# Optimization experiments

Measured on AMD Instinct MI355X. Metric: run time of the kernel, lower is better.

The kernel has to match this reference:

```python
import jax, jax.numpy as jnp
import numpy as np

T, B, F, H, O = 512, 1024, 16, 32, 8  # seq_len, batch, input_size, hidden, classes


def setup_inputs() -> dict:
    key = jax.random.key(0)
    ks = jax.random.split(key, 11)
    s = 1.0 / np.sqrt(H)  # PyTorch LSTM/Linear uniform init scale
    u = lambda k, shp: jax.random.uniform(k, shp, jnp.float32, -s, s)
    return {
        "x": jax.random.normal(ks[0], (T, B, F), jnp.float32),
        "W_ih_f": u(ks[1], (4 * H, F)),
        "W_hh_f": u(ks[2], (4 * H, H)),
        "b_f": u(ks[3], (4 * H,)),  # combined b_ih + b_hh
        "W_ih_b": u(ks[4], (4 * H, F)),
        "W_hh_b": u(ks[5], (4 * H, H)),
        "b_b": u(ks[6], (4 * H,)),
        "W_fc_h": u(ks[7], (O, 2 * H)),
        "b_fc_h": u(ks[8], (O,)),
        "W_fc_o": jax.random.uniform(ks[9], (O, B * O), jnp.float32, -1 / np.sqrt(B * O), 1 / np.sqrt(B * O)),
        "b_fc_o": u(ks[10], (O,)),
    }


def _lstm_final_hidden(x, W_ih, W_hh, b):
    """Run one LSTM direction over x:(T,B,F); return final hidden h:(B,H)."""
    h_dim = W_hh.shape[1]
    # precompute input contribution for all timesteps: (T, B, 4H)
    gates_x = jnp.einsum('tbf,gf->tbg', x, W_ih) + b

    def step(carry, gx):
        h, c = carry
        g = gx + h @ W_hh.T  # (B, 4H), PyTorch gate order i,f,g,o
        i, f, gg, o = jnp.split(g, 4, axis=-1)
        c = jax.nn.sigmoid(f) * c + jax.nn.sigmoid(i) * jnp.tanh(gg)
        h = jax.nn.sigmoid(o) * jnp.tanh(c)
        return (h, c), None

    bsz = x.shape[1]
    init = (jnp.zeros((bsz, h_dim), x.dtype), jnp.zeros((bsz, h_dim), x.dtype))
    (h, _), _ = jax.lax.scan(step, init, gates_x)
    return h


def reference(x, W_ih_f, W_hh_f, b_f, W_ih_b, W_hh_b, b_b,
              W_fc_h, b_fc_h, W_fc_o, b_fc_o):
    h_fwd = _lstm_final_hidden(x, W_ih_f, W_hh_f, b_f)          # hidden_state[-2]
    h_bwd = _lstm_final_hidden(x[::-1], W_ih_b, W_hh_b, b_b)    # hidden_state[-1]
    hidden = jnp.concatenate([h_fwd, h_bwd], axis=1)            # (B, 2H)
    hidden_fc = hidden @ W_fc_h.T + b_fc_h                      # (B, O)
    flat = hidden_fc.reshape(-1)                                # (B*O,) == flat_dim
    out = W_fc_o @ flat + b_fc_o                                # (O,)
    return jax.nn.softmax(out)
```

## Files before the change

kernel.cpp:

```cpp
#include <hip/hip_runtime.h>

#define TT 512
#define BB 1024
#define FF 16
#define HH 32
#define OO 8
#define CH 16
#define NC (TT / CH)
#define NG 128

typedef _Float16 f16;
typedef f16 v2h __attribute__((ext_vector_type(2)));
typedef f16 v4h __attribute__((ext_vector_type(4)));
typedef f16 v8h __attribute__((ext_vector_type(8)));
typedef float f32x4 __attribute__((ext_vector_type(4)));
typedef int   v2i  __attribute__((ext_vector_type(2)));

__device__ __forceinline__ float rcp_fast(float x) { return __builtin_amdgcn_rcpf(x); }
__device__ __forceinline__ float sigm2(float y) {
    return rcp_fast(1.0f + __builtin_amdgcn_exp2f(-y));
}
__device__ __forceinline__ float fdot2(v2h a, v2h b, float c) {
    return __builtin_amdgcn_fdot2(a, b, c, false);
}
__device__ __forceinline__ v2h i2h(int s) { return __builtin_bit_cast(v2h, s); }

__device__ __forceinline__ float xhalf_swap(float v) {
#if __has_builtin(__builtin_amdgcn_permlane32_swap)
    int pi = __float_as_int(v);
    v2i sw = __builtin_amdgcn_permlane32_swap(pi, pi, false, false);
    return __int_as_float(sw.x);
#else
    return __shfl_xor(v, 32);
#endif
}

#define LSTEP(tt)                                                              \
  {                                                                            \
    const int xm = ((tt) & 7) << 2;                                            \
    const float gx0 = gxc[(tt) * NG + (r0 ^ xm)];                              \
    const float gx1 = gxc[(tt) * NG + (r1 ^ xm)];                              \
    float B0 = fdot2(i2h(hs[0]), w0h[0], pb0);                                 \
    float B1 = fdot2(i2h(hs[0]), w1h[0], pb1);                                 \
    float C0 = fdot2(i2h(hs[8]), w0h[8], gx0);                                 \
    float C1 = fdot2(i2h(hs[8]), w1h[8], gx1);                                 \
    _Pragma("unroll")                                                          \
    for (int j = 1; j < 8; ++j) {                                              \
      B0 = fdot2(i2h(hs[j]),     w0h[j],     B0);                              \
      B1 = fdot2(i2h(hs[j]),     w1h[j],     B1);                              \
      C0 = fdot2(i2h(hs[8 + j]), w0h[8 + j], C0);                              \
      C1 = fdot2(i2h(hs[8 + j]), w1h[8 + j], C1);                              \
    }                                                                          \
    const float g0 = B0 + C0;                                                  \
    const float g1 = B1 + C1;                                                  \
    const float s0 = sigm2(g0);                         \
    const float s1 = fmaf(sigm2(g1), pm, pa);           \
    const float prod = s0 * s1;                                                \
    const float recv = xhalf_swap(prod);                                       \
    c = fmaf(s0, c, recv);                               \
    const float th = fmaf(2.0f, sigm2(L2E2 * c), -1.0f);                       \
    h = s1 * th;                                           \
    const int hn = __builtin_amdgcn_mov_dpp(__float_as_int(h),                 \
                                            0xB1, 0xF, 0xF, true);             \
    auto pk = __builtin_amdgcn_cvt_pkrtz(h, __int_as_float(hn));               \
    const int pki = __builtin_bit_cast(int, pk);                               \
    _Pragma("unroll")                                                          \
    for (int m = 0; m < HH / 2; ++m)                                           \
      hs[m] = __builtin_amdgcn_readlane(pki, 32 + 2 * m);                      \
  }

__global__ __launch_bounds__(64, 2)
void lstm_seq_kernel(const float* __restrict__ x,
                     const float* __restrict__ Wih_f, const float* __restrict__ Whh_f,
                     const float* __restrict__ b_f,
                     const float* __restrict__ Wih_b, const float* __restrict__ Whh_b,
                     const float* __restrict__ b_b,
                     float* __restrict__ hidden)
{
    const int bid  = blockIdx.x;
    const int dir  = bid >> 10;
    const int bb   = bid & (BB - 1);
    const int lane = threadIdx.x;
    const int hi   = lane >> 5;
    const int kk   = lane & 31;

    const float* __restrict__ Wih  = dir ? Wih_b : Wih_f;
    const float* __restrict__ Whh  = dir ? Whh_b : Whh_f;
    const float* __restrict__ bias = dir ? b_b   : b_f;

    const float LOG2E = 1.4426950408889634f;
    const float L2E2  = 2.0f * LOG2E;

    const int r0 = kk + hi * HH;
    const int r1 = r0 + 2 * HH;
    const float sc0 = LOG2E;
    const float sc1 = hi ? LOG2E : L2E2;
    const float pm = hi ? 1.0f : 2.0f;
    const float pa = hi ? 0.0f : -1.0f;

    v2h w0h[HH / 2], w1h[HH / 2];
#pragma unroll
    for (int q = 0; q < HH / 4; ++q) {
        float4 a = ((const float4*)(Whh + r0 * HH))[q];
        w0h[2*q]   = (v2h){(f16)(a.x * sc0), (f16)(a.y * sc0)};
        w0h[2*q+1] = (v2h){(f16)(a.z * sc0), (f16)(a.w * sc0)};
        float4 b2 = ((const float4*)(Whh + r1 * HH))[q];
        w1h[2*q]   = (v2h){(f16)(b2.x * sc1), (f16)(b2.y * sc1)};
        w1h[2*q+1] = (v2h){(f16)(b2.z * sc1), (f16)(b2.w * sc1)};
    }
    const float pb0 = bias[r0] * sc0;
    const float pb1 = bias[r1] * sc1;

    v8h awx[8];
#pragma unroll
    for (int T = 0; T < 8; ++T) {
        v8h t = {(f16)0,(f16)0,(f16)0,(f16)0,(f16)0,(f16)0,(f16)0,(f16)0};
        if (lane < 32) {
            const int gate = T * 16 + (lane & 15);
            const float sc = (gate >= 64 && gate < 96) ? L2E2 : LOG2E;
            const float* wrow = Wih + gate * FF + (lane >> 4) * 8;
#pragma unroll
            for (int j = 0; j < 8; ++j) t[j] = (f16)(wrow[j] * sc);
        }
        awx[T] = t;
    }

    __shared__ __align__(16) f16   xsb[2 * CH * FF];
    __shared__ __align__(16) float gxb[2 * CH * NG];

    const int sl = lane >> 2;
    const int wl = lane & 3;
    const int t0 = dir ? (TT - 1 - sl) : sl;
    const float* xp = x + (size_t)t0 * (BB * FF) + (size_t)bb * FF + wl * 4;
    const ptrdiff_t dstep = (dir ? -(ptrdiff_t)CH : (ptrdiff_t)CH) * (BB * FF);

    const int mst = lane & 15;
    const int mq  = (lane >> 4) * 4;
    const int mxr = (mst & 7) << 2;

    {
        float4 f0 = *(const float4*)xp;
        *(v4h*)(xsb + sl * FF + wl * 4) =
            (v4h){(f16)f0.x, (f16)f0.y, (f16)f0.z, (f16)f0.w};
    }
    xp += dstep;
    {
        v8h bx0 = {(f16)0,(f16)0,(f16)0,(f16)0,(f16)0,(f16)0,(f16)0,(f16)0};
        if (lane < 32)
            bx0 = *(const v8h*)(xsb + (lane & 15) * FF + (lane >> 4) * 8);
        float* gw = gxb + mst * NG;
#pragma unroll
        for (int T = 0; T < 8; ++T) {
            f32x4 acc = __builtin_amdgcn_mfma_f32_16x16x32_f16(
                awx[T], bx0, (f32x4){0.f, 0.f, 0.f, 0.f}, 0, 0, 0);
            *(f32x4*)(gw + ((mq + T * 16) ^ mxr)) = acc;
        }
    }
    float4 nf = *(const float4*)xp;
    xp += dstep;

    float c = 0.0f, h = 0.0f;
    int hs[HH / 2];
#pragma unroll
    for (int m = 0; m < HH / 2; ++m) hs[m] = 0;

    for (int ci = 0; ci < NC; ++ci) {
        const int bufc = ci & 1;
        const int bufn = bufc ^ 1;
        const bool more = (ci + 1 < NC);

        v8h bx = {(f16)0,(f16)0,(f16)0,(f16)0,(f16)0,(f16)0,(f16)0,(f16)0};
        if (more) {
            *(v4h*)(xsb + bufn * (CH * FF) + sl * FF + wl * 4) =
                (v4h){(f16)nf.x, (f16)nf.y, (f16)nf.z, (f16)nf.w};
            if (lane < 32)
                bx = *(const v8h*)(xsb + bufn * (CH * FF) + (lane & 15) * FF + (lane >> 4) * 8);
            if (ci + 2 < NC) { nf = *(const float4*)xp; xp += dstep; }
        }

        const float* gxc = gxb + bufc * (CH * NG);

#pragma unroll
        for (int tt = 0; tt < 12; ++tt) LSTEP(tt)

        if (more) {
            float* gw = gxb + bufn * (CH * NG) + mst * NG;
#pragma unroll
            for (int T = 0; T < 8; ++T) {
                f32x4 acc = __builtin_amdgcn_mfma_f32_16x16x32_f16(
                    awx[T], bx, (f32x4){0.f, 0.f, 0.f, 0.f}, 0, 0, 0);
                *(f32x4*)(gw + ((mq + T * 16) ^ mxr)) = acc;
            }
        }

#pragma unroll
        for (int tt = 12; tt < CH; ++tt) LSTEP(tt)
    }

    if (hi) hidden[(size_t)bb * 64 + dir * HH + kk] = h;
}

__global__ __launch_bounds__(256)
void fc_partial_kernel(const float* __restrict__ hidden,
                       const float* __restrict__ Wfh, const float* __restrict__ bfh,
                       const float* __restrict__ Wfo,
                       float* __restrict__ partials)
{
    __shared__ float wsh[OO * 64];
    const int tid = threadIdx.x;
    for (int i = tid; i < OO * 64; i += 256) wsh[i] = Wfh[i];
    __syncthreads();

    const int r   = tid >> 3;
    const int o   = tid & 7;
    const int row = blockIdx.x * 32 + r;

    const float* hrow = hidden + (size_t)row * 64;
    float acc = bfh[o];
#pragma unroll
    for (int j = 0; j < 64; ++j) acc += hrow[j] * wsh[o * 64 + j];

    const int fidx = blockIdx.x * 256 + tid;

    float pv[OO];
#pragma unroll
    for (int o2 = 0; o2 < OO; ++o2) pv[o2] = Wfo[(size_t)o2 * (BB * OO) + fidx] * acc;

    __shared__ float red[4][OO];
#pragma unroll
    for (int o2 = 0; o2 < OO; ++o2) {
        float v = pv[o2];
        for (int off = 32; off > 0; off >>= 1) v += __shfl_down(v, off);
        if ((tid & 63) == 0) red[tid >> 6][o2] = v;
    }
    __syncthreads();
    if (tid < OO) {
        partials[blockIdx.x * OO + tid] =
            red[0][tid] + red[1][tid] + red[2][tid] + red[3][tid];
    }
}

__global__ void finalize_kernel(const float* __restrict__ partials,
                                const float* __restrict__ bfo,
                                float* __restrict__ out)
{
    __shared__ float s[OO];
    const int tid = threadIdx.x;
    if (tid < OO) {
        float acc = bfo[tid];
        for (int b = 0; b < 32; ++b) acc += partials[b * OO + tid];
        s[tid] = acc;
    }
    __syncthreads();
    if (tid == 0) {
        float m = s[0];
        for (int i = 1; i < OO; ++i) m = fmaxf(m, s[i]);
        float e[OO], sum = 0.0f;
        for (int i = 0; i < OO; ++i) { e[i] = expf(s[i] - m); sum += e[i]; }
        for (int i = 0; i < OO; ++i) out[i] = e[i] / sum;
    }
}

extern "C" void kernel_launch(void* const* d_in, const int* in_sizes, int n_in,
                              void* d_out, int out_size, void* d_ws, size_t ws_size,
                              hipStream_t stream) {
    const float* x     = (const float*)d_in[0];
    const float* Wih_f = (const float*)d_in[1];
    const float* Whh_f = (const float*)d_in[2];
    const float* b_f   = (const float*)d_in[3];
    const float* Wih_b = (const float*)d_in[4];
    const float* Whh_b = (const float*)d_in[5];
    const float* b_b   = (const float*)d_in[6];
    const float* Wfh   = (const float*)d_in[7];
    const float* bfh   = (const float*)d_in[8];
    const float* Wfo   = (const float*)d_in[9];
    const float* bfo   = (const float*)d_in[10];

    float* hidden   = (float*)d_ws;
    float* partials = hidden + (size_t)BB * 64;

    lstm_seq_kernel<<<2 * BB, 64, 0, stream>>>(x, Wih_f, Whh_f, b_f,
                                               Wih_b, Whh_b, b_b, hidden);
    fc_partial_kernel<<<32, 256, 0, stream>>>(hidden, Wfh, bfh, Wfo, partials);
    finalize_kernel<<<1, 64, 0, stream>>>(partials, bfo, (float*)d_out);
}
```

Baseline: 178.7 us.

## Interleave two independent batch sequences per wavefront to hide recurrence latency

Each 64-lane block now runs two batch elements (A and B) of the same direction, interleaving their LSTM steps so one chain's dependent operations can fill the other's latency bubbles. The grid is halved to 1024 blocks and launch bounds drop to one wave per EU minimum, allowing more registers for the doubled state (hs arrays, c, h, gate buffers). This trades occupancy and register pressure for instruction-level parallelism on the serial recurrence; shared memory per block also doubles.

```diff
diff --git a/kernel.cpp b/kernel.cpp
--- a/kernel.cpp
+++ b/kernel.cpp
@@ -35,21 +35,21 @@
 #endif
 }
 
-#define LSTEP(tt)                                                              \
+#define LSTEP(tt, S)                                                           \
   {                                                                            \
     const int xm = ((tt) & 7) << 2;                                            \
-    const float gx0 = gxc[(tt) * NG + (r0 ^ xm)];                              \
-    const float gx1 = gxc[(tt) * NG + (r1 ^ xm)];                              \
-    float B0 = fdot2(i2h(hs[0]), w0h[0], pb0);                                 \
-    float B1 = fdot2(i2h(hs[0]), w1h[0], pb1);                                 \
-    float C0 = fdot2(i2h(hs[8]), w0h[8], gx0);                                 \
-    float C1 = fdot2(i2h(hs[8]), w1h[8], gx1);                                 \
+    const float gx0 = gxc##S[(tt) * NG + (r0 ^ xm)];                           \
+    const float gx1 = gxc##S[(tt) * NG + (r1 ^ xm)];                           \
+    float B0 = fdot2(i2h(hs##S[0]), w0h[0], pb0);                              \
+    float B1 = fdot2(i2h(hs##S[0]), w1h[0], pb1);                              \
+    float C0 = fdot2(i2h(hs##S[8]), w0h[8], gx0);                              \
+    float C1 = fdot2(i2h(hs##S[8]), w1h[8], gx1);                              \
     _Pragma("unroll")                                                          \
     for (int j = 1; j < 8; ++j) {                                              \
-      B0 = fdot2(i2h(hs[j]),     w0h[j],     B0);                              \
-      B1 = fdot2(i2h(hs[j]),     w1h[j],     B1);                              \
-      C0 = fdot2(i2h(hs[8 + j]), w0h[8 + j], C0);                              \
-      C1 = fdot2(i2h(hs[8 + j]), w1h[8 + j], C1);                              \
+      B0 = fdot2(i2h(hs##S[j]),     w0h[j],     B0);                           \
+      B1 = fdot2(i2h(hs##S[j]),     w1h[j],     B1);                           \
+      C0 = fdot2(i2h(hs##S[8 + j]), w0h[8 + j], C0);                           \
+      C1 = fdot2(i2h(hs##S[8 + j]), w1h[8 + j], C1);                           \
     }                                                                          \
     const float g0 = B0 + C0;                                                  \
     const float g1 = B1 + C1;                                                  \
@@ -57,19 +57,19 @@
     const float s1 = fmaf(sigm2(g1), pm, pa);           \
     const float prod = s0 * s1;                                                \
     const float recv = xhalf_swap(prod);                                       \
-    c = fmaf(s0, c, recv);                               \
-    const float th = fmaf(2.0f, sigm2(L2E2 * c), -1.0f);                       \
-    h = s1 * th;                                           \
-    const int hn = __builtin_amdgcn_mov_dpp(__float_as_int(h),                 \
+    c##S = fmaf(s0, c##S, recv);                         \
+    const float th = fmaf(2.0f, sigm2(L2E2 * c##S), -1.0f);                    \
+    h##S = s1 * th;                                        \
+    const int hn = __builtin_amdgcn_mov_dpp(__float_as_int(h##S),              \
                                             0xB1, 0xF, 0xF, true);             \
-    auto pk = __builtin_amdgcn_cvt_pkrtz(h, __int_as_float(hn));               \
+    auto pk = __builtin_amdgcn_cvt_pkrtz(h##S, __int_as_float(hn));            \
     const int pki = __builtin_bit_cast(int, pk);                               \
     _Pragma("unroll")                                                          \
     for (int m = 0; m < HH / 2; ++m)                                           \
-      hs[m] = __builtin_amdgcn_readlane(pki, 32 + 2 * m);                      \
+      hs##S[m] = __builtin_amdgcn_readlane(pki, 32 + 2 * m);                   \
   }
 
-__global__ __launch_bounds__(64, 2)
+__global__ __launch_bounds__(64, 1)
 void lstm_seq_kernel(const float* __restrict__ x,
                      const float* __restrict__ Wih_f, const float* __restrict__ Whh_f,
                      const float* __restrict__ b_f,
@@ -78,8 +78,9 @@
                      float* __restrict__ hidden)
 {
     const int bid  = blockIdx.x;
-    const int dir  = bid >> 10;
-    const int bb   = bid & (BB - 1);
+    const int dir  = bid >> 9;
+    const int bbA  = (bid & 511) * 2;
+    const int bbB  = bbA + 1;
     const int lane = threadIdx.x;
     const int hi   = lane >> 5;
     const int kk   = lane & 31;
@@ -125,79 +126,105 @@
         awx[T] = t;
     }
 
-    __shared__ __align__(16) f16   xsb[2 * CH * FF];
-    __shared__ __align__(16) float gxb[2 * CH * NG];
+    __shared__ __align__(16) f16   xsbA[2 * CH * FF], xsbB[2 * CH * FF];
+    __shared__ __align__(16) float gxbA[2 * CH * NG], gxbB[2 * CH * NG];
 
     const int sl = lane >> 2;
     const int wl = lane & 3;
     const int t0 = dir ? (TT - 1 - sl) : sl;
-    const float* xp = x + (size_t)t0 * (BB * FF) + (size_t)bb * FF + wl * 4;
+    const float* xpA = x + (size_t)t0 * (BB * FF) + (size_t)bbA * FF + wl * 4;
+    const float* xpB = x + (size_t)t0 * (BB * FF) + (size_t)bbB * FF + wl * 4;
     const ptrdiff_t dstep = (dir ? -(ptrdiff_t)CH : (ptrdiff_t)CH) * (BB * FF);
 
     const int mst = lane & 15;
     const int mq  = (lane >> 4) * 4;
     const int mxr = (mst & 7) << 2;
+    const int bsel = (lane & 15) * FF + (lane >> 4) * 8;
 
     {
-        float4 f0 = *(const float4*)xp;
-        *(v4h*)(xsb + sl * FF + wl * 4) =
-            (v4h){(f16)f0.x, (f16)f0.y, (f16)f0.z, (f16)f0.w};
-    }
-    xp += dstep;
+        float4 fA = *(const float4*)xpA;
+        float4 fB = *(const float4*)xpB;
+        *(v4h*)(xsbA + sl * FF + wl * 4) =
+            (v4h){(f16)fA.x, (f16)fA.y, (f16)fA.z, (f16)fA.w};
+        *(v4h*)(xsbB + sl * FF + wl * 4) =
+            (v4h){(f16)fB.x, (f16)fB.y, (f16)fB.z, (f16)fB.w};
+    }
+    xpA += dstep; xpB += dstep;
     {
-        v8h bx0 = {(f16)0,(f16)0,(f16)0,(f16)0,(f16)0,(f16)0,(f16)0,(f16)0};
-        if (lane < 32)
-            bx0 = *(const v8h*)(xsb + (lane & 15) * FF + (lane >> 4) * 8);
-        float* gw = gxb + mst * NG;
+        v8h bxA = {(f16)0,(f16)0,(f16)0,(f16)0,(f16)0,(f16)0,(f16)0,(f16)0};
+        v8h bxB = bxA;
+        if (lane < 32) { bxA = *(const v8h*)(xsbA + bsel);
+                         bxB = *(const v8h*)(xsbB + bsel); }
+        float* gwA = gxbA + mst * NG;
+        float* gwB = gxbB + mst * NG;
 #pragma unroll
         for (int T = 0; T < 8; ++T) {
-            f32x4 acc = __builtin_amdgcn_mfma_f32_16x16x32_f16(
-                awx[T], bx0, (f32x4){0.f, 0.f, 0.f, 0.f}, 0, 0, 0);
-            *(f32x4*)(gw + ((mq + T * 16) ^ mxr)) = acc;
+            f32x4 aA = __builtin_amdgcn_mfma_f32_16x16x32_f16(
+                awx[T], bxA, (f32x4){0.f, 0.f, 0.f, 0.f}, 0, 0, 0);
+            f32x4 aB = __builtin_amdgcn_mfma_f32_16x16x32_f16(
+                awx[T], bxB, (f32x4){0.f, 0.f, 0.f, 0.f}, 0, 0, 0);
+            *(f32x4*)(gwA + ((mq + T * 16) ^ mxr)) = aA;
+            *(f32x4*)(gwB + ((mq + T * 16) ^ mxr)) = aB;
         }
     }
-    float4 nf = *(const float4*)xp;
-    xp += dstep;
-
-    float c = 0.0f, h = 0.0f;
-    int hs[HH / 2];
-#pragma unroll
-    for (int m = 0; m < HH / 2; ++m) hs[m] = 0;
+    float4 nfA = *(const float4*)xpA;  xpA += dstep;
+    float4 nfB = *(const float4*)xpB;  xpB += dstep;
+
+    float cA = 0.0f, hA = 0.0f, cB = 0.0f, hB = 0.0f;
+    int hsA[HH / 2], hsB[HH / 2];
+#pragma unroll
+    for (int m = 0; m < HH / 2; ++m) { hsA[m] = 0; hsB[m] = 0; }
 
     for (int ci = 0; ci < NC; ++ci) {
         const int bufc = ci & 1;
         const int bufn = bufc ^ 1;
         const bool more = (ci + 1 < NC);
 
-        v8h bx = {(f16)0,(f16)0,(f16)0,(f16)0,(f16)0,(f16)0,(f16)0,(f16)0};
+        v8h bxA = {(f16)0,(f16)0,(f16)0,(f16)0,(f16)0,(f16)0,(f16)0,(f16)0};
+        v8h bxB = bxA;
         if (more) {
-            *(v4h*)(xsb + bufn * (CH * FF) + sl * FF + wl * 4) =
-                (v4h){(f16)nf.x, (f16)nf.y, (f16)nf.z, (f16)nf.w};
-            if (lane < 32)
-                bx = *(const v8h*)(xsb + bufn * (CH * FF) + (lane & 15) * FF + (lane >> 4) * 8);
-            if (ci + 2 < NC) { nf = *(const float4*)xp; xp += dstep; }
-        }
-
-        const float* gxc = gxb + bufc * (CH * NG);
-
-#pragma unroll
-        for (int tt = 0; tt < 12; ++tt) LSTEP(tt)
-
-        if (more) {
-            float* gw = gxb + bufn * (CH * NG) + mst * NG;
-#pragma unroll
-            for (int T = 0; T < 8; ++T) {
-                f32x4 acc = __builtin_amdgcn_mfma_f32_16x16x32_f16(
-                    awx[T], bx, (f32x4){0.f, 0.f, 0.f, 0.f}, 0, 0, 0);
-                *(f32x4*)(gw + ((mq + T * 16) ^ mxr)) = acc;
+            *(v4h*)(xsbA + bufn * (CH * FF) + sl * FF + wl * 4) =
+                (v4h){(f16)nfA.x, (f16)nfA.y, (f16)nfA.z, (f16)nfA.w};
+            *(v4h*)(xsbB + bufn * (CH * FF) + sl * FF + wl * 4) =
+                (v4h){(f16)nfB.x, (f16)nfB.y, (f16)nfB.z, (f16)nfB.w};
+            if (lane < 32) {
+                bxA = *(const v8h*)(xsbA + bufn * (CH * FF) + bsel);
+                bxB = *(const v8h*)(xsbB + bufn * (CH * FF) + bsel);
+            }
+            if (ci + 2 < NC) {
+                nfA = *(const float4*)xpA;  xpA += dstep;
+                nfB = *(const float4*)xpB;  xpB += dstep;
             }
         }
 
-#pragma unroll
-        for (int tt = 12; tt < CH; ++tt) LSTEP(tt)
-    }
-
-    if (hi) hidden[(size_t)bb * 64 + dir * HH + kk] = h;
+        const float* gxcA = gxbA + bufc * (CH * NG);
+        const float* gxcB = gxbB + bufc * (CH * NG);
+
+#pragma unroll
+        for (int tt = 0; tt < 12; ++tt) { LSTEP(tt, A) LSTEP(tt, B) }
+
+        if (more) {
+            float* gwA = gxbA + bufn * (CH * NG) + mst * NG;
+            float* gwB = gxbB + bufn * (CH * NG) + mst * NG;
+#pragma unroll
+            for (int T = 0; T < 8; ++T) {
+                f32x4 aA = __builtin_amdgcn_mfma_f32_16x16x32_f16(
+                    awx[T], bxA, (f32x4){0.f, 0.f, 0.f, 0.f}, 0, 0, 0);
+                f32x4 aB = __builtin_amdgcn_mfma_f32_16x16x32_f16(
+                    awx[T], bxB, (f32x4){0.f, 0.f, 0.f, 0.f}, 0, 0, 0);
+                *(f32x4*)(gwA + ((mq + T * 16) ^ mxr)) = aA;
+                *(f32x4*)(gwB + ((mq + T * 16) ^ mxr)) = aB;
+            }
+        }
+
+#pragma unroll
+        for (int tt = 12; tt < CH; ++tt) { LSTEP(tt, A) LSTEP(tt, B) }
+    }
+
+    if (hi) {
+        hidden[(size_t)bbA * 64 + dir * HH + kk] = hA;
+        hidden[(size_t)bbB * 64 + dir * HH + kk] = hB;
+    }
 }
 
 __global__ __launch_bounds__(256)
@@ -279,8 +306,8 @@
     float* hidden   = (float*)d_ws;
     float* partials = hidden + (size_t)BB * 64;
 
-    lstm_seq_kernel<<<2 * BB, 64, 0, stream>>>(x, Wih_f, Whh_f, b_f,
-                                               Wih_b, Whh_b, b_b, hidden);
+    lstm_seq_kernel<<<BB, 64, 0, stream>>>(x, Wih_f, Whh_f, b_f,
+                                           Wih_b, Whh_b, b_b, hidden);
     fc_partial_kernel<<<32, 256, 0, stream>>>(hidden, Wfh, bfh, Wfo, partials);
     finalize_kernel<<<1, 64, 0, stream>>>(partials, bfo, (float*)d_out);
 }
```

New measurement: 189.9 us. 6.3% more time.
